# Performance work log

Hardware: AMD Instinct MI355X
Metric: run time of the kernel (lower is better)

## Reference

```python
import jax, jax.numpy as jnp
import numpy as np

B, N, D, H, PD, HID = 16, 512, 512, 8, 9, 32
DH = D // H


def setup_inputs() -> dict:
    key = jax.random.key(0)
    ks = jax.random.split(key, 8)
    h = jax.random.normal(ks[0], (B, N, D), dtype=jnp.float32)
    v = jax.random.normal(ks[1], (B, N, 4), dtype=jnp.float32)
    m = jax.random.randint(ks[2], (B, N), 0, 2, dtype=jnp.int32)
    token_type_ids = jax.random.randint(ks[3], (N,), 0, 4, dtype=jnp.int32)
    s = 1.0 / np.sqrt(D)
    W_qkv = jax.random.normal(ks[4], (D, 3 * D), dtype=jnp.float32) * s
    W_out = jax.random.normal(ks[5], (D, D), dtype=jnp.float32) * s
    W1 = jax.random.normal(ks[6], (PD, HID), dtype=jnp.float32) * (1.0 / np.sqrt(PD))
    b1 = jnp.zeros((HID,), dtype=jnp.float32)
    W2 = jax.random.normal(ks[7], (HID, H), dtype=jnp.float32) * (1.0 / np.sqrt(HID))
    b2 = jnp.zeros((H,), dtype=jnp.float32)
    return {"h": h, "v": v, "m": m, "token_type_ids": token_type_ids,
            "W_qkv": W_qkv, "W_out": W_out, "W1": W1, "b1": b1, "W2": W2, "b2": b2}


def build_pairwise_features(v, token_type_ids):
    # v: [B,N,4] -> e: [B,N,N,9] = [v_i - v_j (4), v_i * v_j (4), same_type (1)]
    vi = v[:, :, None, :]
    vj = v[:, None, :, :]
    same = (token_type_ids[:, None] == token_type_ids[None, :]).astype(v.dtype)
    same = jnp.broadcast_to(same[None, :, :, None], v.shape[:1] + same.shape + (1,))
    return jnp.concatenate([vi - vj, vi * vj, same], axis=-1)


def reference(h, v, m, token_type_ids, W_qkv, W_out, W1, b1, W2, b2):
    Bq, Nq, Dq = h.shape
    qkv = h @ W_qkv                                    # [B,N,3D]
    q, k, vv = jnp.split(qkv, 3, axis=-1)
    def heads(x):
        return x.reshape(Bq, Nq, H, DH).transpose(0, 2, 1, 3)  # [B,H,N,dh]
    q, k, vv = heads(q), heads(k), heads(vv)
    logits = jnp.einsum('bhid,bhjd->bhij', q, k) / jnp.sqrt(jnp.float32(DH))
    e = build_pairwise_features(v, token_type_ids)     # [B,N,N,9]
    bias = jax.nn.relu(e @ W1 + b1) @ W2 + b2          # [B,N,N,H]
    logits = logits + bias.transpose(0, 3, 1, 2)       # [B,H,N,N]
    key_invalid = (m == 0)[:, None, None, :]           # [B,1,1,N]
    logits = jnp.where(key_invalid, -jnp.inf, logits)
    attn = jax.nn.softmax(logits, axis=-1)             # dropout is identity (p=0/eval)
    out = jnp.einsum('bhij,bhjd->bhid', attn, vv)
    out = out.transpose(0, 2, 1, 3).reshape(Bq, Nq, Dq) @ W_out
    out = out * (m != 0).astype(out.dtype)[:, :, None]
    return out
```

## Files before the change

### kernel.cpp

```cpp
#include <hip/hip_runtime.h>
#include <hip/hip_bf16.h>
#include <hip/hip_fp16.h>

#define NN 512
#define HH 8
#define DHH 64

typedef __attribute__((ext_vector_type(8))) short short8v;
typedef __attribute__((ext_vector_type(8))) unsigned short ushort8v;
typedef __attribute__((ext_vector_type(4))) unsigned short ushort4v;
typedef __attribute__((ext_vector_type(4))) float f32x4;
typedef __attribute__((ext_vector_type(8))) _Float16 f16x8;
typedef __attribute__((ext_vector_type(4))) _Float16 f16x4;

__device__ __forceinline__ unsigned short f2bf(float x) {
  unsigned u = __builtin_bit_cast(unsigned, x);
  u += 0x7FFFu + ((u >> 16) & 1u);
  return (unsigned short)(u >> 16);
}
__device__ __forceinline__ int swz64(int r, int cb) { return r * 64 + (cb ^ (((r >> 1) & 3) << 4)); }
__device__ __forceinline__ int swz128(int r, int cb) { return r * 128 + (cb ^ ((r & 7) << 4)); }

__global__ __launch_bounds__(256) void transpose_cvt(const float* __restrict__ src,
                                                     unsigned short* __restrict__ dst,
                                                     int R, int C) {
  __shared__ float t[32][33];
  const int r0 = blockIdx.x * 32, c0 = blockIdx.y * 32;
  const int rr = threadIdx.x >> 3, c4 = (threadIdx.x & 7) * 4;
  float4 v = *(const float4*)&src[(size_t)(r0 + rr) * C + c0 + c4];
  t[rr][c4 + 0] = v.x; t[rr][c4 + 1] = v.y; t[rr][c4 + 2] = v.z; t[rr][c4 + 3] = v.w;
  __syncthreads();
  ushort4v o;
#pragma unroll
  for (int e = 0; e < 4; ++e) o[e] = f2bf(t[c4 + e][rr]);
  *(ushort4v*)&dst[(size_t)(c0 + rr) * R + r0 + c4] = o;
}

template <bool AF32>
__device__ __forceinline__ void gemm128_body(const void* __restrict__ Ap,
                                             const unsigned short* __restrict__ Bt,
                                             int ldk, int m0, int n0,
                                             f32x4 acc[4][4], unsigned char* smem) {
  const int tid = threadIdx.x, lane = tid & 63, wid = tid >> 6;
  const int wm = wid >> 1, wn = wid & 1;
  int aoff[4], boff[4];
#pragma unroll
  for (int i = 0; i < 4; ++i) {
    aoff[i] = swz64(wm * 64 + i * 16 + (lane & 15), (lane >> 4) * 16);
    boff[i] = 8192 + swz64(wn * 64 + i * 16 + (lane & 15), (lane >> 4) * 16);
  }
  for (int k0 = 0; k0 < ldk; k0 += 32) {
#pragma unroll
    for (int p = 0; p < 2; ++p) {
      const int idx = p * 256 + tid;
      const int r = idx >> 2, cg = idx & 3;
      if constexpr (AF32) {
        const float* A = (const float*)Ap;
        const float* ar = &A[(size_t)(m0 + r) * ldk + k0 + cg * 8];
        float4 f0 = *(const float4*)&ar[0];
        float4 f1 = *(const float4*)&ar[4];
        ushort8v av;
        av[0] = f2bf(f0.x); av[1] = f2bf(f0.y); av[2] = f2bf(f0.z); av[3] = f2bf(f0.w);
        av[4] = f2bf(f1.x); av[5] = f2bf(f1.y); av[6] = f2bf(f1.z); av[7] = f2bf(f1.w);
        *(ushort8v*)&smem[swz64(r, cg * 16)] = av;
      } else {
        const unsigned short* A = (const unsigned short*)Ap;
        ushort8v av = *(const ushort8v*)&A[(size_t)(m0 + r) * ldk + k0 + cg * 8];
        *(ushort8v*)&smem[swz64(r, cg * 16)] = av;
      }
      ushort8v bv = *(const ushort8v*)&Bt[(size_t)(n0 + r) * ldk + k0 + cg * 8];
      *(ushort8v*)&smem[8192 + swz64(r, cg * 16)] = bv;
    }
    __syncthreads();
    short8v a[4], b[4];
#pragma unroll
    for (int i = 0; i < 4; ++i) {
      a[i] = *(const short8v*)&smem[aoff[i]];
      b[i] = *(const short8v*)&smem[boff[i]];
    }
#pragma unroll
    for (int i = 0; i < 4; ++i)
#pragma unroll
      for (int j = 0; j < 4; ++j)
        acc[i][j] = __builtin_amdgcn_mfma_f32_16x16x32_bf16(a[i], b[j], acc[i][j], 0, 0, 0);
    __syncthreads();
  }
}

__global__ __launch_bounds__(256) void gemm_qkv(const float* __restrict__ A,
                                                const unsigned short* __restrict__ Bt,
                                                unsigned short* __restrict__ q,
                                                unsigned short* __restrict__ k,
                                                unsigned short* __restrict__ v) {
  __shared__ unsigned char smem[16384];
  f32x4 acc[4][4];
  const f32x4 z = {0.f, 0.f, 0.f, 0.f};
#pragma unroll
  for (int i = 0; i < 4; ++i)
#pragma unroll
    for (int j = 0; j < 4; ++j) acc[i][j] = z;
  gemm128_body<true>(A, Bt, 512, blockIdx.x * 128, blockIdx.y * 128, acc, smem);
  const int lane = threadIdx.x & 63, wid = threadIdx.x >> 6;
  const int wm = wid >> 1, wn = wid & 1;
#pragma unroll
  for (int i = 0; i < 4; ++i) {
    const int row0 = blockIdx.x * 128 + wm * 64 + i * 16 + ((lane >> 4) << 2);
#pragma unroll
    for (int j = 0; j < 4; ++j) {
      const int col = blockIdx.y * 128 + wn * 64 + j * 16 + (lane & 15);
      const int part = col >> 9, head = (col >> 6) & 7, dh = col & 63;
      unsigned short* dst = (part == 0) ? q : ((part == 1) ? k : v);
#pragma unroll
      for (int rr = 0; rr < 4; ++rr) {
        const int row = row0 + rr;
        const int b_ = row >> 9, n_ = row & 511;
        dst[(((b_ * HH + head) * NN) + n_) * DHH + dh] = f2bf(acc[i][j][rr]);
      }
    }
  }
}

__global__ __launch_bounds__(256) void gemm_out(const unsigned short* __restrict__ A,
                                                const unsigned short* __restrict__ Bt,
                                                const int* __restrict__ msk,
                                                float* __restrict__ out) {
  __shared__ unsigned char smem[16384];
  f32x4 acc[4][4];
  const f32x4 z = {0.f, 0.f, 0.f, 0.f};
#pragma unroll
  for (int i = 0; i < 4; ++i)
#pragma unroll
    for (int j = 0; j < 4; ++j) acc[i][j] = z;
  gemm128_body<false>(A, Bt, 512, blockIdx.x * 128, blockIdx.y * 128, acc, smem);
  const int lane = threadIdx.x & 63, wid = threadIdx.x >> 6;
  const int wm = wid >> 1, wn = wid & 1;
#pragma unroll
  for (int i = 0; i < 4; ++i) {
    const int row0 = blockIdx.x * 128 + wm * 64 + i * 16 + ((lane >> 4) << 2);
#pragma unroll
    for (int j = 0; j < 4; ++j) {
      const int col = blockIdx.y * 128 + wn * 64 + j * 16 + (lane & 15);
#pragma unroll
      for (int rr = 0; rr < 4; ++rr) {
        const int row = row0 + rr;
        const float mm = (msk[row] != 0) ? 1.f : 0.f;
        out[(size_t)row * 512 + col] = acc[i][j][rr] * mm;
      }
    }
  }
}

__global__ __launch_bounds__(256) void bias_mlp_mfma(
    const float* __restrict__ v, const int* __restrict__ tti,
    const float* __restrict__ W1, const float* __restrict__ b1,
    const float* __restrict__ W2, const float* __restrict__ b2,
    __half* __restrict__ bias) {
  __shared__ float sv[NN][4];
  __shared__ int stt[NN];
  __shared__ _Float16 hbuf[4][2][16 * 40];
  const int tid = threadIdx.x, lane = tid & 63, w = tid >> 6;
  const int i = blockIdx.x, b = blockIdx.y;
  const int l16 = lane & 15, lg = lane >> 4;
  for (int idx = tid; idx < NN; idx += 256) {
    *(float4*)&sv[idx][0] = *(const float4*)&v[(b * NN + idx) * 4];
    stt[idx] = tti[idx];
  }
  f16x8 w1f[2], w2f;
#pragma unroll
  for (int t = 0; t < 2; ++t)
#pragma unroll
    for (int e = 0; e < 8; ++e) {
      const int kk = lg * 8 + e;
      w1f[t][e] = (kk < 9) ? (_Float16)W1[kk * 32 + t * 16 + l16] : (_Float16)0.f;
    }
#pragma unroll
  for (int e = 0; e < 8; ++e)
    w2f[e] = (l16 < 8) ? (_Float16)W2[(lg * 8 + e) * 8 + l16] : (_Float16)0.f;
  const float b1v0 = b1[l16], b1v1 = b1[16 + l16];
  const float b2v = (l16 < 8) ? b2[l16] : 0.f;
  __syncthreads();
  const float4 vi = *(const float4*)&sv[i][0];
  const int ti = stt[i];
  int bsel = 0;
#pragma unroll 2
  for (int j0 = w * 16; j0 < NN; j0 += 64) {
    _Float16* hb = &hbuf[w][bsel][0];
    const int j = j0 + l16;
    const float4 vj = *(const float4*)&sv[j][0];
    f16x8 af = {0, 0, 0, 0, 0, 0, 0, 0};
    if (lg == 0) {
      af[0] = (_Float16)(vi.x - vj.x); af[1] = (_Float16)(vi.y - vj.y);
      af[2] = (_Float16)(vi.z - vj.z); af[3] = (_Float16)(vi.w - vj.w);
      af[4] = (_Float16)(vi.x * vj.x); af[5] = (_Float16)(vi.y * vj.y);
      af[6] = (_Float16)(vi.z * vj.z); af[7] = (_Float16)(vi.w * vj.w);
    } else if (lg == 1) {
      af[0] = (ti == stt[j]) ? (_Float16)1.f : (_Float16)0.f;
    }
    f32x4 h0 = {b1v0, b1v0, b1v0, b1v0};
    f32x4 h1 = {b1v1, b1v1, b1v1, b1v1};
    h0 = __builtin_amdgcn_mfma_f32_16x16x32_f16(af, w1f[0], h0, 0, 0, 0);
    h1 = __builtin_amdgcn_mfma_f32_16x16x32_f16(af, w1f[1], h1, 0, 0, 0);
#pragma unroll
    for (int r = 0; r < 4; ++r) {
      const int row = lg * 4 + r;
      hb[row * 40 + l16] = (_Float16)fmaxf(h0[r], 0.f);
      hb[row * 40 + 16 + l16] = (_Float16)fmaxf(h1[r], 0.f);
    }
    f16x8 af2 = *(const f16x8*)&hb[l16 * 40 + lg * 8];
    f32x4 o = {b2v, b2v, b2v, b2v};
    o = __builtin_amdgcn_mfma_f32_16x16x32_f16(af2, w2f, o, 0, 0, 0);
    if (l16 < 8) {
      f16x4 pk;
#pragma unroll
      for (int r = 0; r < 4; ++r) pk[r] = (_Float16)o[r];
      *(f16x4*)&bias[((size_t)(b * HH + l16) * NN + i) * NN + j0 + lg * 4] = pk;
    }
    bsel ^= 1;
  }
}

__global__ __launch_bounds__(256) void attn_mfma(
    const unsigned short* __restrict__ q, const unsigned short* __restrict__ k,
    const unsigned short* __restrict__ v, const __half* __restrict__ bias,
    const int* __restrict__ msk, unsigned short* __restrict__ ao) {
  __shared__ unsigned char vt[8192];
  __shared__ unsigned char ps[4][2048];
  __shared__ float smask[NN];
  const int tid = threadIdx.x, lane = tid & 63, w = tid >> 6;
  const int it = blockIdx.x, h_ = blockIdx.y, b_ = blockIdx.z;
  const int bh = b_ * HH + h_;
  const unsigned short* qb = q + ((size_t)bh * NN + it * 64) * DHH;
  const unsigned short* kb = k + (size_t)bh * NN * DHH;
  const unsigned short* vb = v + (size_t)bh * NN * DHH;
  const __half* bb = bias + (size_t)bh * NN * NN;
  for (int j = tid; j < NN; j += 256) smask[j] = (msk[b_ * NN + j] != 0) ? 0.f : -1e30f;
  short8v qf[2];
#pragma unroll
  for (int kc = 0; kc < 2; ++kc)
    qf[kc] = *(const short8v*)&qb[(w * 16 + (lane & 15)) * DHH + kc * 32 + (lane >> 4) * 8];
  f32x4 acc[4];
  const f32x4 z = {0.f, 0.f, 0.f, 0.f};
#pragma unroll
  for (int d = 0; d < 4; ++d) acc[d] = z;
  float mrow[4], lrow[4];
#pragma unroll
  for (int r = 0; r < 4; ++r) { mrow[r] = -1e30f; lrow[r] = 0.f; }
  __syncthreads();
  const int irow_base = it * 64 + w * 16 + ((lane >> 4) << 2);
  for (int j0 = 0; j0 < NN; j0 += 64) {
#pragma unroll
    for (int p = 0; p < 2; ++p) {
      const int idx = p * 256 + tid;
      const int j = idx & 63, dh0 = (idx >> 6) * 8;
      ushort8v v8 = *(const ushort8v*)&vb[(j0 + j) * DHH + dh0];
#pragma unroll
      for (int e = 0; e < 8; ++e)
        *(unsigned short*)&vt[swz128(dh0 + e, 2 * j)] = v8[e];
    }
    f32x4 s[4];
#pragma unroll
    for (int jt = 0; jt < 4; ++jt) {
      const unsigned short* kr = &kb[(j0 + jt * 16 + (lane & 15)) * DHH + (lane >> 4) * 8];
      short8v kf0 = *(const short8v*)&kr[0];
      short8v kf1 = *(const short8v*)&kr[32];
      f32x4 t = z;
      t = __builtin_amdgcn_mfma_f32_16x16x32_bf16(qf[0], kf0, t, 0, 0, 0);
      t = __builtin_amdgcn_mfma_f32_16x16x32_bf16(qf[1], kf1, t, 0, 0, 0);
      s[jt] = t;
    }
#pragma unroll
    for (int jt = 0; jt < 4; ++jt) {
      const int jcol = j0 + jt * 16 + (lane & 15);
#pragma unroll
      for (int r = 0; r < 4; ++r) {
        const float bv = __half2float(bb[(size_t)(irow_base + r) * NN + jcol]);
        s[jt][r] = fmaf(s[jt][r], 0.125f, bv) + smask[jcol];
      }
    }
    float alpha[4];
#pragma unroll
    for (int r = 0; r < 4; ++r) {
      float tm = fmaxf(fmaxf(s[0][r], s[1][r]), fmaxf(s[2][r], s[3][r]));
      tm = fmaxf(tm, __shfl_xor(tm, 1));
      tm = fmaxf(tm, __shfl_xor(tm, 2));
      tm = fmaxf(tm, __shfl_xor(tm, 4));
      tm = fmaxf(tm, __shfl_xor(tm, 8));
      const float mn = fmaxf(mrow[r], tm);
      alpha[r] = __expf(mrow[r] - mn);
      mrow[r] = mn;
      float ts = 0.f;
#pragma unroll
      for (int jt = 0; jt < 4; ++jt) {
        const float p = __expf(s[jt][r] - mn);
        s[jt][r] = p;
        ts += p;
      }
      ts += __shfl_xor(ts, 1);
      ts += __shfl_xor(ts, 2);
      ts += __shfl_xor(ts, 4);
      ts += __shfl_xor(ts, 8);
      lrow[r] = lrow[r] * alpha[r] + ts;
    }
#pragma unroll
    for (int d = 0; d < 4; ++d)
#pragma unroll
      for (int r = 0; r < 4; ++r) acc[d][r] *= alpha[r];
#pragma unroll
    for (int jt = 0; jt < 4; ++jt)
#pragma unroll
      for (int r = 0; r < 4; ++r)
        *(unsigned short*)&ps[w][swz128(((lane >> 4) << 2) + r, jt * 32 + 2 * (lane & 15))] =
            f2bf(s[jt][r]);
    __syncthreads();
    short8v pf[2];
#pragma unroll
    for (int kc = 0; kc < 2; ++kc)
      pf[kc] = *(const short8v*)&ps[w][swz128(lane & 15, kc * 64 + (lane >> 4) * 16)];
#pragma unroll
    for (int d = 0; d < 4; ++d) {
      short8v vf0 = *(const short8v*)&vt[swz128(d * 16 + (lane & 15), (lane >> 4) * 16)];
      short8v vf1 = *(const short8v*)&vt[swz128(d * 16 + (lane & 15), 64 + (lane >> 4) * 16)];
      acc[d] = __builtin_amdgcn_mfma_f32_16x16x32_bf16(pf[0], vf0, acc[d], 0, 0, 0);
      acc[d] = __builtin_amdgcn_mfma_f32_16x16x32_bf16(pf[1], vf1, acc[d], 0, 0, 0);
    }
    __syncthreads();
  }
#pragma unroll
  for (int d = 0; d < 4; ++d) {
#pragma unroll
    for (int r = 0; r < 4; ++r) {
      const int row = irow_base + r;
      ao[(size_t)(b_ * NN + row) * 512 + h_ * DHH + d * 16 + (lane & 15)] =
          f2bf(acc[d][r] / lrow[r]);
    }
  }
}

extern "C" void kernel_launch(void* const* d_in, const int* in_sizes, int n_in,
                              void* d_out, int out_size, void* d_ws, size_t ws_size,
                              hipStream_t stream) {
  const float* h     = (const float*)d_in[0];
  const float* v     = (const float*)d_in[1];
  const int*   m     = (const int*)d_in[2];
  const int*   tti   = (const int*)d_in[3];
  const float* W_qkv = (const float*)d_in[4];
  const float* W_out = (const float*)d_in[5];
  const float* W1    = (const float*)d_in[6];
  const float* b1    = (const float*)d_in[7];
  const float* W2    = (const float*)d_in[8];
  const float* b2    = (const float*)d_in[9];
  float* out = (float*)d_out;
  unsigned char* ws = (unsigned char*)d_ws;

  unsigned short* q_bf  = (unsigned short*)(ws + 8388608);
  unsigned short* k_bf  = (unsigned short*)(ws + 16777216);
  unsigned short* v_bf  = (unsigned short*)(ws + 25165824);
  unsigned short* ao_bf = (unsigned short*)(ws + 33554432);
  unsigned short* WqT   = (unsigned short*)(ws + 41943040);
  unsigned short* WoT   = (unsigned short*)(ws + 43515904);
  __half* bias          = (__half*)(ws + 44040192);

  transpose_cvt<<<dim3(16, 48), 256, 0, stream>>>(W_qkv, WqT, 512, 1536);
  transpose_cvt<<<dim3(16, 16), 256, 0, stream>>>(W_out, WoT, 512, 512);
  gemm_qkv<<<dim3(64, 12), 256, 0, stream>>>(h, WqT, q_bf, k_bf, v_bf);
  bias_mlp_mfma<<<dim3(512, 16), 256, 0, stream>>>(v, tti, W1, b1, W2, b2, bias);
  attn_mfma<<<dim3(8, 8, 16), 256, 0, stream>>>(q_bf, k_bf, v_bf, bias, m, ao_bf);
  gemm_out<<<dim3(64, 4), 256, 0, stream>>>(ao_bf, WoT, m, out);
}
```

Baseline: 152.8 us.

## Store V transposed from QKV GEMM and batch 8 query rows per bias block

The QKV GEMM epilogue now writes V in a [B,H,DH,N] transposed layout with packed 4-element stores. The attention kernel can then load V tiles with vector reads and one vector LDS store each, replacing the scalar scatter-transpose. Separately, the bias MLP kernel processes 8 query rows per block, cutting the grid 8x so v/tti staging and weight setup are amortised. The hbuf double buffer is dropped, which may add LDS hazards, though each wave uses its own buffer region.

Result: no change. 155.4 us (+1.7%).

```diff
diff --git a/kernel.cpp b/kernel.cpp
--- a/kernel.cpp
+++ b/kernel.cpp
@@ -91,7 +91,7 @@
                                                 const unsigned short* __restrict__ Bt,
                                                 unsigned short* __restrict__ q,
                                                 unsigned short* __restrict__ k,
-                                                unsigned short* __restrict__ v) {
+                                                unsigned short* __restrict__ vt) {
   __shared__ unsigned char smem[16384];
   f32x4 acc[4][4];
   const f32x4 z = {0.f, 0.f, 0.f, 0.f};
@@ -109,12 +109,20 @@
     for (int j = 0; j < 4; ++j) {
       const int col = blockIdx.y * 128 + wn * 64 + j * 16 + (lane & 15);
       const int part = col >> 9, head = (col >> 6) & 7, dh = col & 63;
-      unsigned short* dst = (part == 0) ? q : ((part == 1) ? k : v);
-#pragma unroll
-      for (int rr = 0; rr < 4; ++rr) {
-        const int row = row0 + rr;
-        const int b_ = row >> 9, n_ = row & 511;
-        dst[(((b_ * HH + head) * NN) + n_) * DHH + dh] = f2bf(acc[i][j][rr]);
+      if (part == 2) {
+        const int b_ = row0 >> 9, n_ = row0 & 511;
+        ushort4v pk;
+#pragma unroll
+        for (int rr = 0; rr < 4; ++rr) pk[rr] = f2bf(acc[i][j][rr]);
+        *(ushort4v*)&vt[(((b_ * HH + head) * DHH) + dh) * NN + n_] = pk;
+      } else {
+        unsigned short* dst = (part == 0) ? q : k;
+#pragma unroll
+        for (int rr = 0; rr < 4; ++rr) {
+          const int row = row0 + rr;
+          const int b_ = row >> 9, n_ = row & 511;
+          dst[(((b_ * HH + head) * NN) + n_) * DHH + dh] = f2bf(acc[i][j][rr]);
+        }
       }
     }
   }
@@ -157,9 +165,9 @@
     __half* __restrict__ bias) {
   __shared__ float sv[NN][4];
   __shared__ int stt[NN];
-  __shared__ _Float16 hbuf[4][2][16 * 40];
+  __shared__ _Float16 hbuf[4][16 * 40];
   const int tid = threadIdx.x, lane = tid & 63, w = tid >> 6;
-  const int i = blockIdx.x, b = blockIdx.y;
+  const int i0 = blockIdx.x * 8, b = blockIdx.y;
   const int l16 = lane & 15, lg = lane >> 4;
   for (int idx = tid; idx < NN; idx += 256) {
     *(float4*)&sv[idx][0] = *(const float4*)&v[(b * NN + idx) * 4];
@@ -179,49 +187,49 @@
   const float b1v0 = b1[l16], b1v1 = b1[16 + l16];
   const float b2v = (l16 < 8) ? b2[l16] : 0.f;
   __syncthreads();
-  const float4 vi = *(const float4*)&sv[i][0];
-  const int ti = stt[i];
-  int bsel = 0;
-#pragma unroll 2
-  for (int j0 = w * 16; j0 < NN; j0 += 64) {
-    _Float16* hb = &hbuf[w][bsel][0];
-    const int j = j0 + l16;
-    const float4 vj = *(const float4*)&sv[j][0];
-    f16x8 af = {0, 0, 0, 0, 0, 0, 0, 0};
-    if (lg == 0) {
-      af[0] = (_Float16)(vi.x - vj.x); af[1] = (_Float16)(vi.y - vj.y);
-      af[2] = (_Float16)(vi.z - vj.z); af[3] = (_Float16)(vi.w - vj.w);
-      af[4] = (_Float16)(vi.x * vj.x); af[5] = (_Float16)(vi.y * vj.y);
-      af[6] = (_Float16)(vi.z * vj.z); af[7] = (_Float16)(vi.w * vj.w);
-    } else if (lg == 1) {
-      af[0] = (ti == stt[j]) ? (_Float16)1.f : (_Float16)0.f;
-    }
-    f32x4 h0 = {b1v0, b1v0, b1v0, b1v0};
-    f32x4 h1 = {b1v1, b1v1, b1v1, b1v1};
-    h0 = __builtin_amdgcn_mfma_f32_16x16x32_f16(af, w1f[0], h0, 0, 0, 0);
-    h1 = __builtin_amdgcn_mfma_f32_16x16x32_f16(af, w1f[1], h1, 0, 0, 0);
-#pragma unroll
-    for (int r = 0; r < 4; ++r) {
-      const int row = lg * 4 + r;
-      hb[row * 40 + l16] = (_Float16)fmaxf(h0[r], 0.f);
-      hb[row * 40 + 16 + l16] = (_Float16)fmaxf(h1[r], 0.f);
-    }
-    f16x8 af2 = *(const f16x8*)&hb[l16 * 40 + lg * 8];
-    f32x4 o = {b2v, b2v, b2v, b2v};
-    o = __builtin_amdgcn_mfma_f32_16x16x32_f16(af2, w2f, o, 0, 0, 0);
-    if (l16 < 8) {
-      f16x4 pk;
-#pragma unroll
-      for (int r = 0; r < 4; ++r) pk[r] = (_Float16)o[r];
-      *(f16x4*)&bias[((size_t)(b * HH + l16) * NN + i) * NN + j0 + lg * 4] = pk;
-    }
-    bsel ^= 1;
+  _Float16* hb = &hbuf[w][0];
+  for (int il = 0; il < 8; ++il) {
+    const int i = i0 + il;
+    const float4 vi = *(const float4*)&sv[i][0];
+    const int ti = stt[i];
+    for (int j0 = w * 16; j0 < NN; j0 += 64) {
+      const int j = j0 + l16;
+      const float4 vj = *(const float4*)&sv[j][0];
+      f16x8 af = {0, 0, 0, 0, 0, 0, 0, 0};
+      if (lg == 0) {
+        af[0] = (_Float16)(vi.x - vj.x); af[1] = (_Float16)(vi.y - vj.y);
+        af[2] = (_Float16)(vi.z - vj.z); af[3] = (_Float16)(vi.w - vj.w);
+        af[4] = (_Float16)(vi.x * vj.x); af[5] = (_Float16)(vi.y * vj.y);
+        af[6] = (_Float16)(vi.z * vj.z); af[7] = (_Float16)(vi.w * vj.w);
+      } else if (lg == 1) {
+        af[0] = (ti == stt[j]) ? (_Float16)1.f : (_Float16)0.f;
+      }
+      f32x4 h0 = {b1v0, b1v0, b1v0, b1v0};
+      f32x4 h1 = {b1v1, b1v1, b1v1, b1v1};
+      h0 = __builtin_amdgcn_mfma_f32_16x16x32_f16(af, w1f[0], h0, 0, 0, 0);
+      h1 = __builtin_amdgcn_mfma_f32_16x16x32_f16(af, w1f[1], h1, 0, 0, 0);
+#pragma unroll
+      for (int r = 0; r < 4; ++r) {
+        const int row = lg * 4 + r;
+        hb[row * 40 + l16] = (_Float16)fmaxf(h0[r], 0.f);
+        hb[row * 40 + 16 + l16] = (_Float16)fmaxf(h1[r], 0.f);
+      }
+      f16x8 af2 = *(const f16x8*)&hb[l16 * 40 + lg * 8];
+      f32x4 o = {b2v, b2v, b2v, b2v};
+      o = __builtin_amdgcn_mfma_f32_16x16x32_f16(af2, w2f, o, 0, 0, 0);
+      if (l16 < 8) {
+        f16x4 pk;
+#pragma unroll
+        for (int r = 0; r < 4; ++r) pk[r] = (_Float16)o[r];
+        *(f16x4*)&bias[((size_t)(b * HH + l16) * NN + i) * NN + j0 + lg * 4] = pk;
+      }
+    }
   }
 }
 
 __global__ __launch_bounds__(256) void attn_mfma(
     const unsigned short* __restrict__ q, const unsigned short* __restrict__ k,
-    const unsigned short* __restrict__ v, const __half* __restrict__ bias,
+    const unsigned short* __restrict__ vtg, const __half* __restrict__ bias,
     const int* __restrict__ msk, unsigned short* __restrict__ ao) {
   __shared__ unsigned char vt[8192];
   __shared__ unsigned char ps[4][2048];
@@ -231,7 +239,7 @@
   const int bh = b_ * HH + h_;
   const unsigned short* qb = q + ((size_t)bh * NN + it * 64) * DHH;
   const unsigned short* kb = k + (size_t)bh * NN * DHH;
-  const unsigned short* vb = v + (size_t)bh * NN * DHH;
+  const unsigned short* vb = vtg + (size_t)bh * DHH * NN;
   const __half* bb = bias + (size_t)bh * NN * NN;
   for (int j = tid; j < NN; j += 256) smask[j] = (msk[b_ * NN + j] != 0) ? 0.f : -1e30f;
   short8v qf[2];
@@ -251,11 +259,9 @@
 #pragma unroll
     for (int p = 0; p < 2; ++p) {
       const int idx = p * 256 + tid;
-      const int j = idx & 63, dh0 = (idx >> 6) * 8;
-      ushort8v v8 = *(const ushort8v*)&vb[(j0 + j) * DHH + dh0];
-#pragma unroll
-      for (int e = 0; e < 8; ++e)
-        *(unsigned short*)&vt[swz128(dh0 + e, 2 * j)] = v8[e];
+      const int dh = idx >> 3, jg = idx & 7;
+      ushort8v v8 = *(const ushort8v*)&vb[(size_t)dh * NN + j0 + jg * 8];
+      *(ushort8v*)&vt[swz128(dh, jg * 16)] = v8;
     }
     f32x4 s[4];
 #pragma unroll
@@ -354,7 +360,7 @@
 
   unsigned short* q_bf  = (unsigned short*)(ws + 8388608);
   unsigned short* k_bf  = (unsigned short*)(ws + 16777216);
-  unsigned short* v_bf  = (unsigned short*)(ws + 25165824);
+  unsigned short* vt_bf = (unsigned short*)(ws + 25165824);
   unsigned short* ao_bf = (unsigned short*)(ws + 33554432);
   unsigned short* WqT   = (unsigned short*)(ws + 41943040);
   unsigned short* WoT   = (unsigned short*)(ws + 43515904);
@@ -362,8 +368,8 @@
 
   transpose_cvt<<<dim3(16, 48), 256, 0, stream>>>(W_qkv, WqT, 512, 1536);
   transpose_cvt<<<dim3(16, 16), 256, 0, stream>>>(W_out, WoT, 512, 512);
-  gemm_qkv<<<dim3(64, 12), 256, 0, stream>>>(h, WqT, q_bf, k_bf, v_bf);
-  bias_mlp_mfma<<<dim3(512, 16), 256, 0, stream>>>(v, tti, W1, b1, W2, b2, bias);
-  attn_mfma<<<dim3(8, 8, 16), 256, 0, stream>>>(q_bf, k_bf, v_bf, bias, m, ao_bf);
+  gemm_qkv<<<dim3(64, 12), 256, 0, stream>>>(h, WqT, q_bf, k_bf, vt_bf);
+  bias_mlp_mfma<<<dim3(64, 16), 256, 0, stream>>>(v, tti, W1, b1, W2, b2, bias);
+  attn_mfma<<<dim3(8, 8, 16), 256, 0, stream>>>(q_bf, k_bf, vt_bf, bias, m, ao_bf);
   gemm_out<<<dim3(64, 4), 256, 0, stream>>>(ao_bf, WoT, m, out);
 }
```
